# Optimization experiments

Measured on AMD Instinct MI355X. Metric: run time of the kernel, lower is better.

The kernel has to match this reference:

```python
import jax, jax.numpy as jnp
import numpy as np

B, N, H, W = 8, 16384, 64, 64
CTX, OUT, ST = 32, 2, 1
HID = [516, 256, 128, 64, 32, 16]
IN_SIZE = CTX + 2 + ST + OUT  # 37


def _bilinear_sample(img, coord):
    """torch F.grid_sample, mode=bilinear, padding=zeros, align_corners=False.
    img: [B,C,H,W]; coord: [B,N,2] (x,y in [-1,1]). Returns [B,C,N]."""
    _, _, Hh, Ww = img.shape
    gx = (coord[..., 0] + 1.0) * (Ww * 0.5) - 0.5
    gy = (coord[..., 1] + 1.0) * (Hh * 0.5) - 0.5
    x0 = jnp.floor(gx)
    y0 = jnp.floor(gy)
    wx1 = gx - x0
    wy1 = gy - y0

    def tap(xi, yi, w):
        valid = (xi >= 0) & (xi < Ww) & (yi >= 0) & (yi < Hh)
        xc = jnp.clip(xi, 0, Ww - 1).astype(jnp.int32)
        yc = jnp.clip(yi, 0, Hh - 1).astype(jnp.int32)
        vals = jax.vmap(lambda im, y, x: im[:, y, x])(img, yc, xc)  # [B,C,N]
        return vals * (w * valid)[:, None, :]

    return (tap(x0, y0, (1 - wx1) * (1 - wy1))
            + tap(x0 + 1, y0, wx1 * (1 - wy1))
            + tap(x0, y0 + 1, (1 - wx1) * wy1)
            + tap(x0 + 1, y0 + 1, wx1 * wy1))


def _layer_shapes():
    shapes = [(IN_SIZE, HID[0])]
    for i in range(len(HID) - 1):
        shapes.append((HID[i] + IN_SIZE, HID[i + 1]))
    shapes.append((HID[-1], OUT))
    return shapes


def setup_inputs():
    key = jax.random.key(0)
    ks = jax.random.split(key, 4 + 7)
    inp = {
        "lr_fields": jax.random.normal(ks[0], (B, OUT, H, W), jnp.float32),
        "context_grid": jax.random.normal(ks[1], (B, CTX, H, W), jnp.float32),
        "hr_eps": jax.random.normal(ks[2], (B, H, W), jnp.float32),
        "coord": jax.random.uniform(ks[3], (B, N, 2), jnp.float32, -1.0, 1.0),
    }
    for j, (fi, fo) in enumerate(_layer_shapes()):
        inp[f"W{j}"] = jax.random.normal(ks[4 + j], (fi, fo), jnp.float32) / np.sqrt(fi)
        inp[f"b{j}"] = jnp.zeros((fo,), jnp.float32)
    return inp


def reference(lr_fields, context_grid, hr_eps, coord,
              W0, b0, W1, b1, W2, b2, W3, b3, W4, b4, W5, b5, W6, b6):
    # original permutes (0,1,3,2) before grid_sample -> swap spatial axes
    ctx_pts = _bilinear_sample(jnp.swapaxes(context_grid, 2, 3), coord)  # [B,CTX,N]
    lr_pts = _bilinear_sample(jnp.swapaxes(lr_fields, 2, 3), coord)      # [B,OUT,N]
    eps_pts = _bilinear_sample(jnp.swapaxes(hr_eps[:, None], 2, 3), coord)  # [B,1,N]
    x_in = jnp.concatenate([
        jnp.transpose(ctx_pts, (0, 2, 1)),
        coord,
        jnp.transpose(lr_pts, (0, 2, 1)),
        jnp.transpose(eps_pts, (0, 2, 1)),
    ], axis=2)  # [B,N,37]
    x = jax.nn.relu(x_in @ W0 + b0)
    for Wl, bl in ((W1, b1), (W2, b2), (W3, b3), (W4, b4), (W5, b5)):
        x = jax.nn.relu(jnp.concatenate([x, x_in], axis=2) @ Wl + bl)
    return x @ W6 + b6  # [B,N,2]
```

## Files before the change

kernel.cpp:

```cpp
#include <hip/hip_runtime.h>


#define NTH     1024
#define NWAVES  16
#define MPTS    32
#define MTILES  (MPTS / 16)
#define SROW    872
#define XIN_OFF 0
#define HA_OFF  64
#define HB_OFF  608
#define NPOINTS (8 * 16384)
#define GRIDX   (NPOINTS / MPTS)
#define LDSBYTES (MPTS * SROW * 2)

#define SGB __builtin_amdgcn_sched_group_barrier
#define SG_MFMA   0x008
#define SG_VMREAD 0x020
#define SG_DSREAD 0x100

typedef short          short8  __attribute__((ext_vector_type(8)));
typedef short          short4v __attribute__((ext_vector_type(4)));
typedef float          f32x4   __attribute__((ext_vector_type(4)));
typedef unsigned short u16;

__device__ __forceinline__ u16 f2bf(float f) {
    unsigned int u = __builtin_bit_cast(unsigned int, f);
    u += 0x7fffu + ((u >> 16) & 1u);
    return (u16)(u >> 16);
}

__constant__ int pk_base8[8] = {0, 4224, 23680, 28800, 30336, 30848, 31040, 31104};
__constant__ int pk_ks[7]    = {2, 19, 10, 6, 4, 3, 1};
__constant__ int pk_khp[7]   = {0, 544, 256, 128, 64, 32, 32};
__constant__ int pk_kact[7]  = {0, 516, 256, 128, 64, 32, 16};
__constant__ int pk_nact[7]  = {516, 256, 128, 64, 32, 16, 2};

struct WPtrs { const float* W[7]; };

__global__ void pack_weights(WPtrs wp, u16* __restrict__ out)
{
    const int f = blockIdx.x * blockDim.x + threadIdx.x;
    if (f >= 31104) return;
    int l = 0;
    while (l < 6 && f >= pk_base8[l + 1]) ++l;
    const int r    = f - pk_base8[l];
    const int lane = r & 63;
    const int t    = r >> 6;
    const int ks   = pk_ks[l];
    const int s    = t % ks;
    const int nt   = t / ks;
    const int n    = nt * 16 + (lane & 15);
    const int k0   = s * 32 + (lane >> 4) * 8;
    const int nact = pk_nact[l];
    const int khp  = pk_khp[l];
    const int kact = pk_kact[l];
    const float* W = wp.W[l];

    union { short8 v; u16 e[8]; } frag;
#pragma unroll
    for (int j = 0; j < 8; ++j) {
        const int k = k0 + j;
        float v = 0.0f;
        if (n < nact) {
            if (k < khp) {
                if (k < kact) v = W[k * nact + n];
            } else {
                const int xr = k - khp;
                if (xr < 37) v = W[(kact + xr) * nact + n];
            }
        }
        frag.e[j] = f2bf(v);
    }
    *(short8*)(out + (size_t)f * 8) = frag.v;
}

template<int KHP, int HSEG, int OSEG, int NT, int NACT, int LBASE,
         bool XIN, bool RELU, bool GOUT>
__device__ __forceinline__ void mlayer(const u16* __restrict__ wpack,
                                       const float* __restrict__ bias,
                                       u16* __restrict__ s_act,
                                       float* __restrict__ gout, int p0,
                                       int wave, int lane)
{
    constexpr int KHS = KHP / 32;
    constexpr int KS  = KHS + (XIN ? 2 : 0);
    constexpr int MS  = MTILES;
    const int lm = lane & 15;
    const int lq = lane >> 4;
    const u16* wl = wpack + LBASE + lane * 8;

    const u16* arow[MS];
#pragma unroll
    for (int m = 0; m < MS; ++m)
        arow[m] = s_act + (m * 16 + lm) * SROW + lq * 8;

    for (int nt = wave; nt < NT; nt += NWAVES) {
        const u16* bp = wl + (size_t)nt * KS * 512;

        f32x4 acc[MS];
#pragma unroll
        for (int m = 0; m < MS; ++m)
            acc[m] = (f32x4){0.f, 0.f, 0.f, 0.f};

#pragma unroll
        for (int s = 0; s < KS; ++s) {
            const int ab = (s < KHS) ? (HSEG + s * 32)
                                     : (XIN_OFF + (s - KHS) * 32);
            short8 a[MS];
#pragma unroll
            for (int m = 0; m < MS; ++m)
                a[m] = *(const short8*)(arow[m] + ab);
            const short8 b = *(const short8*)(bp + (size_t)s * 512);
#pragma unroll
            for (int m = 0; m < MS; ++m)
                acc[m] = __builtin_amdgcn_mfma_f32_16x16x32_bf16(b, a[m], acc[m], 0, 0, 0);
        }

        SGB(SG_DSREAD, 2, 0); SGB(SG_VMREAD, 1, 0);
        if (KS > 1) { SGB(SG_DSREAD, 2, 0); SGB(SG_VMREAD, 1, 0); }
#pragma unroll
        for (int s = 0; s < KS; ++s) {
            SGB(SG_MFMA, 2, 0);
            if (s + 2 < KS) { SGB(SG_DSREAD, 2, 0); SGB(SG_VMREAD, 1, 0); }
        }

        const int bn = nt * 16 + lq * 4;
        float bv[4];
        if (bn + 4 <= NACT) {
            const f32x4 b4 = *(const f32x4*)(bias + bn);
            bv[0] = b4[0]; bv[1] = b4[1]; bv[2] = b4[2]; bv[3] = b4[3];
        } else {
#pragma unroll
            for (int r = 0; r < 4; ++r)
                bv[r] = (bn + r < NACT) ? bias[bn + r] : 0.f;
        }
        if (GOUT) {
            if (lq == 0) {
#pragma unroll
                for (int m = 0; m < MS; ++m) {
                    float2 o;
                    o.x = acc[m][0] + bv[0];
                    o.y = acc[m][1] + bv[1];
                    *(float2*)(gout + (size_t)(p0 + m * 16 + lm) * 2) = o;
                }
            }
        } else {
#pragma unroll
            for (int m = 0; m < MS; ++m) {
                short4v o;
#pragma unroll
                for (int r = 0; r < 4; ++r) {
                    float v = acc[m][r] + bv[r];
                    if (RELU) v = fmaxf(v, 0.f);
                    o[r] = (short)f2bf(v);
                }
                *(short4v*)(s_act + (size_t)(m * 16 + lm) * SROW + OSEG + bn) = o;
            }
        }
    }
}

struct MainParams {
    const float* lr;
    const float* ctx;
    const float* eps;
    const float* coord;
    const float* Bb[7];
    const u16*   wpack;
    float*       out;
};

__global__ __launch_bounds__(NTH, 8)
void cont_decoder_mfma(MainParams p)
{
    extern __shared__ u16 s_act[];
    __shared__ int   s_x0[MPTS], s_y0[MPTS];
    __shared__ float s_wx[MPTS], s_wy[MPTS];

    const int tid  = threadIdx.x;
    const int wave = tid >> 6;
    const int lane = tid & 63;
    const int p0   = blockIdx.x * MPTS;
    const int b    = p0 >> 14;

    for (int i = tid; i < MPTS * 43; i += NTH) {
        const int pt = i / 43, c = i % 43;
        const int col = (c < 27) ? (37 + c) : (592 + (c - 27));
        s_act[pt * SROW + col] = 0;
    }

    if (tid < MPTS) {
        const int pt = p0 + tid;
        const float cx = p.coord[2 * pt];
        const float cy = p.coord[2 * pt + 1];
        const float gx = (cx + 1.0f) * 32.0f - 0.5f;
        const float gy = (cy + 1.0f) * 32.0f - 0.5f;
        const float fx0 = floorf(gx), fy0 = floorf(gy);
        s_x0[tid] = (int)fx0;
        s_y0[tid] = (int)fy0;
        s_wx[tid] = gx - fx0;
        s_wy[tid] = gy - fy0;
        s_act[tid * SROW + 32] = f2bf(cx);
        s_act[tid * SROW + 33] = f2bf(cy);
    }
    __syncthreads();

    for (int idx = tid; idx < MPTS * 35; idx += NTH) {
        const int t = idx / 35;
        const int c = idx % 35;
        const float* base;
        int col;
        if (c < 32)      { base = p.ctx + (size_t)(b * 32 + c) * 4096;       col = c; }
        else if (c < 34) { base = p.lr  + (size_t)(b * 2 + (c - 32)) * 4096; col = 34 + (c - 32); }
        else             { base = p.eps + (size_t)b * 4096;                   col = 36; }

        const int   x0 = s_x0[t], y0 = s_y0[t];
        const float wx = s_wx[t], wy = s_wy[t];
        const int x1 = x0 + 1, y1 = y0 + 1;
        const bool xv0 = (x0 >= 0) & (x0 < 64);
        const bool xv1 = (x1 >= 0) & (x1 < 64);
        const bool yv0 = (y0 >= 0) & (y0 < 64);
        const bool yv1 = (y1 >= 0) & (y1 < 64);
        const int xc0 = min(max(x0, 0), 63), xc1 = min(max(x1, 0), 63);
        const int yc0 = min(max(y0, 0), 63), yc1 = min(max(y1, 0), 63);

        const float w00 = (1.0f - wx) * (1.0f - wy) * ((xv0 && yv0) ? 1.0f : 0.0f);
        const float w10 = wx * (1.0f - wy)          * ((xv1 && yv0) ? 1.0f : 0.0f);
        const float w01 = (1.0f - wx) * wy          * ((xv0 && yv1) ? 1.0f : 0.0f);
        const float w11 = wx * wy                   * ((xv1 && yv1) ? 1.0f : 0.0f);

        const float val = w00 * base[xc0 * 64 + yc0]
                        + w10 * base[xc1 * 64 + yc0]
                        + w01 * base[xc0 * 64 + yc1]
                        + w11 * base[xc1 * 64 + yc1];
        s_act[t * SROW + col] = f2bf(val);
    }
    __syncthreads();

    mlayer<  0,  HA_OFF, HA_OFF, 33, 516, 0,      true,  true,  false>(p.wpack, p.Bb[0], s_act, nullptr, p0, wave, lane);
    __syncthreads();
    mlayer<544,  HA_OFF, HB_OFF, 16, 256, 33792,  true,  true,  false>(p.wpack, p.Bb[1], s_act, nullptr, p0, wave, lane);
    __syncthreads();
    mlayer<256,  HB_OFF, HA_OFF,  8, 128, 189440, true,  true,  false>(p.wpack, p.Bb[2], s_act, nullptr, p0, wave, lane);
    __syncthreads();
    mlayer<128,  HA_OFF, HB_OFF,  4,  64, 230400, true,  true,  false>(p.wpack, p.Bb[3], s_act, nullptr, p0, wave, lane);
    __syncthreads();
    mlayer< 64,  HB_OFF, HA_OFF,  2,  32, 242688, true,  true,  false>(p.wpack, p.Bb[4], s_act, nullptr, p0, wave, lane);
    __syncthreads();
    mlayer< 32,  HA_OFF, HB_OFF,  1,  16, 246784, true,  true,  false>(p.wpack, p.Bb[5], s_act, nullptr, p0, wave, lane);
    __syncthreads();
    mlayer< 32,  HB_OFF, 0,       1,   2, 248320, false, false, true >(p.wpack, p.Bb[6], s_act, p.out,   p0, wave, lane);
}

extern "C" void kernel_launch(void* const* d_in, const int* in_sizes, int n_in,
                              void* d_out, int out_size, void* d_ws, size_t ws_size,
                              hipStream_t stream)
{
    WPtrs wp;
    for (int l = 0; l < 7; ++l) wp.W[l] = (const float*)d_in[4 + 2 * l];

    MainParams p;
    p.lr    = (const float*)d_in[0];
    p.ctx   = (const float*)d_in[1];
    p.eps   = (const float*)d_in[2];
    p.coord = (const float*)d_in[3];
    for (int l = 0; l < 7; ++l) p.Bb[l] = (const float*)d_in[5 + 2 * l];
    p.wpack = (const u16*)d_ws;
    p.out   = (float*)d_out;

    hipFuncSetAttribute((const void*)cont_decoder_mfma,
                        hipFuncAttributeMaxDynamicSharedMemorySize, LDSBYTES);

    hipLaunchKernelGGL(pack_weights, dim3(122), dim3(256), 0, stream, wp, (u16*)d_ws);
    hipLaunchKernelGGL(cont_decoder_mfma, dim3(GRIDX), dim3(NTH), LDSBYTES, stream, p);
}
```

Measured before the change: 220.8 us.

## Split K across wave halves for layers 1-2 with LDS partial-sum reduction

For the 256- and 128-wide layers, which had fewer N-tiles than waves and left half the waves idle, the K dimension is now split across two groups of eight waves. Each wave owns NT/8 column tiles, the second group writes fp32 partial sums into an unused LDS region, and the first group adds them, applies bias and ReLU, and stores bf16 activations. The manual sched_group_barrier interleaving hints are also removed. This costs extra barriers, LDS scratch traffic and more accumulator registers per wave.

```diff
diff --git a/kernel.cpp b/kernel.cpp
--- a/kernel.cpp
+++ b/kernel.cpp
@@ -6,17 +6,13 @@
 #define MPTS    32
 #define MTILES  (MPTS / 16)
 #define SROW    872
+#define SROWB   (SROW * 2)
 #define XIN_OFF 0
 #define HA_OFF  64
 #define HB_OFF  608
 #define NPOINTS (8 * 16384)
 #define GRIDX   (NPOINTS / MPTS)
 #define LDSBYTES (MPTS * SROW * 2)
-
-#define SGB __builtin_amdgcn_sched_group_barrier
-#define SG_MFMA   0x008
-#define SG_VMREAD 0x020
-#define SG_DSREAD 0x100
 
 typedef short          short8  __attribute__((ext_vector_type(8)));
 typedef short          short4v __attribute__((ext_vector_type(4)));
@@ -75,7 +71,7 @@
 }
 
 template<int KHP, int HSEG, int OSEG, int NT, int NACT, int LBASE,
-         bool XIN, bool RELU, bool GOUT>
+         int KSPLIT, int SCRB, bool BAR1, bool XIN, bool RELU, bool GOUT>
 __device__ __forceinline__ void mlayer(const u16* __restrict__ wpack,
                                        const float* __restrict__ bias,
                                        u16* __restrict__ s_act,
@@ -94,67 +90,149 @@
     for (int m = 0; m < MS; ++m)
         arow[m] = s_act + (m * 16 + lm) * SROW + lq * 8;
 
-    for (int nt = wave; nt < NT; nt += NWAVES) {
-        const u16* bp = wl + (size_t)nt * KS * 512;
-
-        f32x4 acc[MS];
-#pragma unroll
-        for (int m = 0; m < MS; ++m)
-            acc[m] = (f32x4){0.f, 0.f, 0.f, 0.f};
-
-#pragma unroll
-        for (int s = 0; s < KS; ++s) {
-            const int ab = (s < KHS) ? (HSEG + s * 32)
-                                     : (XIN_OFF + (s - KHS) * 32);
-            short8 a[MS];
+    if constexpr (KSPLIT == 1) {
+        for (int nt = wave; nt < NT; nt += NWAVES) {
+            const u16* bp = wl + (size_t)nt * KS * 512;
+
+            f32x4 acc[MS];
 #pragma unroll
             for (int m = 0; m < MS; ++m)
-                a[m] = *(const short8*)(arow[m] + ab);
-            const short8 b = *(const short8*)(bp + (size_t)s * 512);
+                acc[m] = (f32x4){0.f, 0.f, 0.f, 0.f};
+
+#pragma unroll
+            for (int s = 0; s < KS; ++s) {
+                const int ab = (s < KHS) ? (HSEG + s * 32)
+                                         : (XIN_OFF + (s - KHS) * 32);
+                short8 a[MS];
+#pragma unroll
+                for (int m = 0; m < MS; ++m)
+                    a[m] = *(const short8*)(arow[m] + ab);
+                const short8 b = *(const short8*)(bp + (size_t)s * 512);
+#pragma unroll
+                for (int m = 0; m < MS; ++m)
+                    acc[m] = __builtin_amdgcn_mfma_f32_16x16x32_bf16(b, a[m], acc[m], 0, 0, 0);
+            }
+
+            const int bn = nt * 16 + lq * 4;
+            float bv[4];
+            if (bn + 4 <= NACT) {
+                const f32x4 b4 = *(const f32x4*)(bias + bn);
+                bv[0] = b4[0]; bv[1] = b4[1]; bv[2] = b4[2]; bv[3] = b4[3];
+            } else {
+#pragma unroll
+                for (int r = 0; r < 4; ++r)
+                    bv[r] = (bn + r < NACT) ? bias[bn + r] : 0.f;
+            }
+            if (GOUT) {
+                if (lq == 0) {
+#pragma unroll
+                    for (int m = 0; m < MS; ++m) {
+                        float2 o;
+                        o.x = acc[m][0] + bv[0];
+                        o.y = acc[m][1] + bv[1];
+                        *(float2*)(gout + (size_t)(p0 + m * 16 + lm) * 2) = o;
+                    }
+                }
+            } else {
+#pragma unroll
+                for (int m = 0; m < MS; ++m) {
+                    short4v o;
+#pragma unroll
+                    for (int r = 0; r < 4; ++r) {
+                        float v = acc[m][r] + bv[r];
+                        if (RELU) v = fmaxf(v, 0.f);
+                        o[r] = (short)f2bf(v);
+                    }
+                    *(short4v*)(s_act + (size_t)(m * 16 + lm) * SROW + OSEG + bn) = o;
+                }
+            }
+        }
+    } else {
+        constexpr int NTN  = NT / 8;
+        constexpr int SMID = (KS + 1) / 2;
+        const int q  = wave & 7;
+        const int kh = wave >> 3;
+
+        const u16* bp[NTN];
+#pragma unroll
+        for (int i = 0; i < NTN; ++i)
+            bp[i] = wl + (size_t)(q + 8 * i) * KS * 512;
+
+        f32x4 acc[NTN][MS];
+#pragma unroll
+        for (int i = 0; i < NTN; ++i)
 #pragma unroll
             for (int m = 0; m < MS; ++m)
-                acc[m] = __builtin_amdgcn_mfma_f32_16x16x32_bf16(b, a[m], acc[m], 0, 0, 0);
-        }
-
-        SGB(SG_DSREAD, 2, 0); SGB(SG_VMREAD, 1, 0);
-        if (KS > 1) { SGB(SG_DSREAD, 2, 0); SGB(SG_VMREAD, 1, 0); }
-#pragma unroll
-        for (int s = 0; s < KS; ++s) {
-            SGB(SG_MFMA, 2, 0);
-            if (s + 2 < KS) { SGB(SG_DSREAD, 2, 0); SGB(SG_VMREAD, 1, 0); }
-        }
-
-        const int bn = nt * 16 + lq * 4;
-        float bv[4];
-        if (bn + 4 <= NACT) {
-            const f32x4 b4 = *(const f32x4*)(bias + bn);
-            bv[0] = b4[0]; bv[1] = b4[1]; bv[2] = b4[2]; bv[3] = b4[3];
+                acc[i][m] = (f32x4){0.f, 0.f, 0.f, 0.f};
+
+#define KSTEP(s_) { \
+            const int ab = ((s_) < KHS) ? (HSEG + (s_) * 32) \
+                                        : (XIN_OFF + ((s_) - KHS) * 32); \
+            short8 a[MS]; \
+            for (int m = 0; m < MS; ++m) \
+                a[m] = *(const short8*)(arow[m] + ab); \
+            for (int i = 0; i < NTN; ++i) { \
+                const short8 b = *(const short8*)(bp[i] + (size_t)(s_) * 512); \
+                for (int m = 0; m < MS; ++m) \
+                    acc[i][m] = __builtin_amdgcn_mfma_f32_16x16x32_bf16(b, a[m], acc[i][m], 0, 0, 0); \
+            } }
+
+        if (kh == 0) {
+#pragma unroll
+            for (int s = 0; s < SMID; ++s) KSTEP(s)
         } else {
 #pragma unroll
-            for (int r = 0; r < 4; ++r)
-                bv[r] = (bn + r < NACT) ? bias[bn + r] : 0.f;
-        }
-        if (GOUT) {
-            if (lq == 0) {
+            for (int s = SMID; s < KS; ++s) KSTEP(s)
+        }
+#undef KSTEP
+
+        if constexpr (BAR1) __syncthreads();
+        if (kh == 1) {
+#pragma unroll
+            for (int i = 0; i < NTN; ++i) {
+                const int nt = q + 8 * i;
 #pragma unroll
                 for (int m = 0; m < MS; ++m) {
-                    float2 o;
-                    o.x = acc[m][0] + bv[0];
-                    o.y = acc[m][1] + bv[1];
-                    *(float2*)(gout + (size_t)(p0 + m * 16 + lm) * 2) = o;
-                }
-            }
-        } else {
-#pragma unroll
-            for (int m = 0; m < MS; ++m) {
-                short4v o;
-#pragma unroll
-                for (int r = 0; r < 4; ++r) {
-                    float v = acc[m][r] + bv[r];
-                    if (RELU) v = fmaxf(v, 0.f);
-                    o[r] = (short)f2bf(v);
-                }
-                *(short4v*)(s_act + (size_t)(m * 16 + lm) * SROW + OSEG + bn) = o;
+                    char* sp = (char*)s_act + (size_t)(m * 16 + lm) * SROWB
+                             + SCRB + nt * 64 + lq * 16;
+                    *(f32x4*)sp = acc[i][m];
+                }
+            }
+        }
+        __syncthreads();
+        if (kh == 0) {
+#pragma unroll
+            for (int i = 0; i < NTN; ++i) {
+                const int nt = q + 8 * i;
+#pragma unroll
+                for (int m = 0; m < MS; ++m) {
+                    const char* sp = (const char*)s_act
+                                   + (size_t)(m * 16 + lm) * SROWB
+                                   + SCRB + nt * 64 + lq * 16;
+                    acc[i][m] += *(const f32x4*)sp;
+                }
+
+                const int bn = nt * 16 + lq * 4;
+                float bv[4];
+                if (bn + 4 <= NACT) {
+                    const f32x4 b4 = *(const f32x4*)(bias + bn);
+                    bv[0] = b4[0]; bv[1] = b4[1]; bv[2] = b4[2]; bv[3] = b4[3];
+                } else {
+#pragma unroll
+                    for (int r = 0; r < 4; ++r)
+                        bv[r] = (bn + r < NACT) ? bias[bn + r] : 0.f;
+                }
+#pragma unroll
+                for (int m = 0; m < MS; ++m) {
+                    short4v o;
+#pragma unroll
+                    for (int r = 0; r < 4; ++r) {
+                        float v = acc[i][m][r] + bv[r];
+                        if (RELU) v = fmaxf(v, 0.f);
+                        o[r] = (short)f2bf(v);
+                    }
+                    *(short4v*)(s_act + (size_t)(m * 16 + lm) * SROW + OSEG + bn) = o;
+                }
             }
         }
     }
@@ -237,19 +315,19 @@
     }
     __syncthreads();
 
-    mlayer<  0,  HA_OFF, HA_OFF, 33, 516, 0,      true,  true,  false>(p.wpack, p.Bb[0], s_act, nullptr, p0, wave, lane);
-    __syncthreads();
-    mlayer<544,  HA_OFF, HB_OFF, 16, 256, 33792,  true,  true,  false>(p.wpack, p.Bb[1], s_act, nullptr, p0, wave, lane);
-    __syncthreads();
-    mlayer<256,  HB_OFF, HA_OFF,  8, 128, 189440, true,  true,  false>(p.wpack, p.Bb[2], s_act, nullptr, p0, wave, lane);
-    __syncthreads();
-    mlayer<128,  HA_OFF, HB_OFF,  4,  64, 230400, true,  true,  false>(p.wpack, p.Bb[3], s_act, nullptr, p0, wave, lane);
-    __syncthreads();
-    mlayer< 64,  HB_OFF, HA_OFF,  2,  32, 242688, true,  true,  false>(p.wpack, p.Bb[4], s_act, nullptr, p0, wave, lane);
-    __syncthreads();
-    mlayer< 32,  HA_OFF, HB_OFF,  1,  16, 246784, true,  true,  false>(p.wpack, p.Bb[5], s_act, nullptr, p0, wave, lane);
-    __syncthreads();
-    mlayer< 32,  HB_OFF, 0,       1,   2, 248320, false, false, true >(p.wpack, p.Bb[6], s_act, p.out,   p0, wave, lane);
+    mlayer<  0,  HA_OFF, HA_OFF, 33, 516, 0,      1,  0,    false, true,  true,  false>(p.wpack, p.Bb[0], s_act, nullptr, p0, wave, lane);
+    __syncthreads();
+    mlayer<544,  HA_OFF, HB_OFF, 16, 256, 33792,  2,  128,  true,  true,  true,  false>(p.wpack, p.Bb[1], s_act, nullptr, p0, wave, lane);
+    __syncthreads();
+    mlayer<256,  HB_OFF, HA_OFF,  8, 128, 189440, 2,  640,  false, true,  true,  false>(p.wpack, p.Bb[2], s_act, nullptr, p0, wave, lane);
+    __syncthreads();
+    mlayer<128,  HA_OFF, HB_OFF,  4,  64, 230400, 1,  0,    false, true,  true,  false>(p.wpack, p.Bb[3], s_act, nullptr, p0, wave, lane);
+    __syncthreads();
+    mlayer< 64,  HB_OFF, HA_OFF,  2,  32, 242688, 1,  0,    false, true,  true,  false>(p.wpack, p.Bb[4], s_act, nullptr, p0, wave, lane);
+    __syncthreads();
+    mlayer< 32,  HA_OFF, HB_OFF,  1,  16, 246784, 1,  0,    false, true,  true,  false>(p.wpack, p.Bb[5], s_act, nullptr, p0, wave, lane);
+    __syncthreads();
+    mlayer< 32,  HB_OFF, 0,       1,   2, 248320, 1,  0,    false, false, false, true >(p.wpack, p.Bb[6], s_act, p.out,   p0, wave, lane);
 }
 
 extern "C" void kernel_launch(void* const* d_in, const int* in_sizes, int n_in,
```

Measured after the change: 225.4 us. 2.1% more time.

## Switch MLP layers from 16x16x32 to 32x32x16 bf16 MFMA with repacked weights

Applied to the files above, without the earlier changes.

Replaces the two 16x16x32 MFMAs per K-step (one per 16-point M tile) with a single 32x32x16 MFMA covering all 32 points and 32 output columns. The weight packing and layer offsets are redone for 32-column fragments with 16-wide K slices, and the manual sched_group_barrier hints are removed. This halves the number of N tiles per layer, which reduces redundant LDS A reads and per-tile epilogue work. The cost is more padding waste on small layers (e.g. the 16- and 2-wide outputs), fewer N tiles to spread across 16 waves, and dropping the explicit instruction interleaving.

```diff
diff --git a/kernel.cpp b/kernel.cpp
--- a/kernel.cpp
+++ b/kernel.cpp
@@ -4,7 +4,6 @@
 #define NTH     1024
 #define NWAVES  16
 #define MPTS    32
-#define MTILES  (MPTS / 16)
 #define SROW    872
 #define XIN_OFF 0
 #define HA_OFF  64
@@ -13,14 +12,10 @@
 #define GRIDX   (NPOINTS / MPTS)
 #define LDSBYTES (MPTS * SROW * 2)
 
-#define SGB __builtin_amdgcn_sched_group_barrier
-#define SG_MFMA   0x008
-#define SG_VMREAD 0x020
-#define SG_DSREAD 0x100
-
 typedef short          short8  __attribute__((ext_vector_type(8)));
 typedef short          short4v __attribute__((ext_vector_type(4)));
 typedef float          f32x4   __attribute__((ext_vector_type(4)));
+typedef float          f32x16  __attribute__((ext_vector_type(16)));
 typedef unsigned short u16;
 
 __device__ __forceinline__ u16 f2bf(float f) {
@@ -29,34 +24,34 @@
     return (u16)(u >> 16);
 }
 
-__constant__ int pk_base8[8] = {0, 4224, 23680, 28800, 30336, 30848, 31040, 31104};
-__constant__ int pk_ks[7]    = {2, 19, 10, 6, 4, 3, 1};
-__constant__ int pk_khp[7]   = {0, 544, 256, 128, 64, 32, 32};
-__constant__ int pk_kact[7]  = {0, 516, 256, 128, 64, 32, 16};
-__constant__ int pk_nact[7]  = {516, 256, 128, 64, 32, 16, 2};
+__constant__ int pk_base[8] = {0, 68, 372, 452, 476, 484, 490, 492};
+__constant__ int pk_ks[7]   = {4, 38, 20, 12, 8, 6, 2};
+__constant__ int pk_khp[7]  = {0, 544, 256, 128, 64, 32, 32};
+__constant__ int pk_kact[7] = {0, 516, 256, 128, 64, 32, 16};
+__constant__ int pk_nact[7] = {516, 256, 128, 64, 32, 16, 2};
 
 struct WPtrs { const float* W[7]; };
 
 __global__ void pack_weights(WPtrs wp, u16* __restrict__ out)
 {
-    const int f = blockIdx.x * blockDim.x + threadIdx.x;
-    if (f >= 31104) return;
+    const int t = blockIdx.x * blockDim.x + threadIdx.x;
+    if (t >= 492 * 64) return;
+    const int frag = t >> 6;
+    const int lane = t & 63;
     int l = 0;
-    while (l < 6 && f >= pk_base8[l + 1]) ++l;
-    const int r    = f - pk_base8[l];
-    const int lane = r & 63;
-    const int t    = r >> 6;
+    while (l < 6 && frag >= pk_base[l + 1]) ++l;
+    const int r    = frag - pk_base[l];
     const int ks   = pk_ks[l];
-    const int s    = t % ks;
-    const int nt   = t / ks;
-    const int n    = nt * 16 + (lane & 15);
-    const int k0   = s * 32 + (lane >> 4) * 8;
+    const int s    = r % ks;
+    const int nt   = r / ks;
+    const int n    = nt * 32 + (lane & 31);
+    const int k0   = s * 16 + (lane >> 5) * 8;
     const int nact = pk_nact[l];
     const int khp  = pk_khp[l];
     const int kact = pk_kact[l];
     const float* W = wp.W[l];
 
-    union { short8 v; u16 e[8]; } frag;
+    union { short8 v; u16 e[8]; } fr;
 #pragma unroll
     for (int j = 0; j < 8; ++j) {
         const int k = k0 + j;
@@ -69,9 +64,9 @@
                 if (xr < 37) v = W[(kact + xr) * nact + n];
             }
         }
-        frag.e[j] = f2bf(v);
-    }
-    *(short8*)(out + (size_t)f * 8) = frag.v;
+        fr.e[j] = f2bf(v);
+    }
+    *(short8*)(out + (size_t)t * 8) = fr.v;
 }
 
 template<int KHP, int HSEG, int OSEG, int NT, int NACT, int LBASE,
@@ -82,79 +77,57 @@
                                        float* __restrict__ gout, int p0,
                                        int wave, int lane)
 {
-    constexpr int KHS = KHP / 32;
-    constexpr int KS  = KHS + (XIN ? 2 : 0);
-    constexpr int MS  = MTILES;
-    const int lm = lane & 15;
-    const int lq = lane >> 4;
-    const u16* wl = wpack + LBASE + lane * 8;
-
-    const u16* arow[MS];
-#pragma unroll
-    for (int m = 0; m < MS; ++m)
-        arow[m] = s_act + (m * 16 + lm) * SROW + lq * 8;
+    constexpr int KHS = KHP / 16;
+    constexpr int KS  = KHS + (XIN ? 4 : 0);
+    const int pt = lane & 31;
+    const int hl = lane >> 5;
+    const u16* wl   = wpack + LBASE + lane * 8;
+    const u16* arow = s_act + pt * SROW + hl * 8;
 
     for (int nt = wave; nt < NT; nt += NWAVES) {
         const u16* bp = wl + (size_t)nt * KS * 512;
 
-        f32x4 acc[MS];
-#pragma unroll
-        for (int m = 0; m < MS; ++m)
-            acc[m] = (f32x4){0.f, 0.f, 0.f, 0.f};
+        f32x16 acc;
+#pragma unroll
+        for (int i = 0; i < 16; ++i) acc[i] = 0.f;
 
 #pragma unroll
         for (int s = 0; s < KS; ++s) {
-            const int ab = (s < KHS) ? (HSEG + s * 32)
-                                     : (XIN_OFF + (s - KHS) * 32);
-            short8 a[MS];
-#pragma unroll
-            for (int m = 0; m < MS; ++m)
-                a[m] = *(const short8*)(arow[m] + ab);
+            const int ab = (s < KHS) ? (HSEG + s * 16)
+                                     : (XIN_OFF + (s - KHS) * 16);
+            const short8 a = *(const short8*)(arow + ab);
             const short8 b = *(const short8*)(bp + (size_t)s * 512);
-#pragma unroll
-            for (int m = 0; m < MS; ++m)
-                acc[m] = __builtin_amdgcn_mfma_f32_16x16x32_bf16(b, a[m], acc[m], 0, 0, 0);
+            acc = __builtin_amdgcn_mfma_f32_32x32x16_bf16(b, a, acc, 0, 0, 0);
         }
 
-        SGB(SG_DSREAD, 2, 0); SGB(SG_VMREAD, 1, 0);
-        if (KS > 1) { SGB(SG_DSREAD, 2, 0); SGB(SG_VMREAD, 1, 0); }
-#pragma unroll
-        for (int s = 0; s < KS; ++s) {
-            SGB(SG_MFMA, 2, 0);
-            if (s + 2 < KS) { SGB(SG_DSREAD, 2, 0); SGB(SG_VMREAD, 1, 0); }
-        }
-
-        const int bn = nt * 16 + lq * 4;
-        float bv[4];
-        if (bn + 4 <= NACT) {
-            const f32x4 b4 = *(const f32x4*)(bias + bn);
-            bv[0] = b4[0]; bv[1] = b4[1]; bv[2] = b4[2]; bv[3] = b4[3];
-        } else {
-#pragma unroll
-            for (int r = 0; r < 4; ++r)
-                bv[r] = (bn + r < NACT) ? bias[bn + r] : 0.f;
-        }
         if (GOUT) {
-            if (lq == 0) {
-#pragma unroll
-                for (int m = 0; m < MS; ++m) {
-                    float2 o;
-                    o.x = acc[m][0] + bv[0];
-                    o.y = acc[m][1] + bv[1];
-                    *(float2*)(gout + (size_t)(p0 + m * 16 + lm) * 2) = o;
-                }
+            if (hl == 0) {
+                float2 o;
+                o.x = acc[0] + bias[0];
+                o.y = acc[1] + bias[1];
+                *(float2*)(gout + (size_t)(p0 + pt) * 2) = o;
             }
         } else {
 #pragma unroll
-            for (int m = 0; m < MS; ++m) {
+            for (int rq = 0; rq < 4; ++rq) {
+                const int bn = nt * 32 + rq * 8 + hl * 4;
+                float bv[4];
+                if (bn + 4 <= NACT) {
+                    const f32x4 b4 = *(const f32x4*)(bias + bn);
+                    bv[0] = b4[0]; bv[1] = b4[1]; bv[2] = b4[2]; bv[3] = b4[3];
+                } else {
+#pragma unroll
+                    for (int e = 0; e < 4; ++e)
+                        bv[e] = (bn + e < NACT) ? bias[bn + e] : 0.f;
+                }
                 short4v o;
 #pragma unroll
-                for (int r = 0; r < 4; ++r) {
-                    float v = acc[m][r] + bv[r];
+                for (int e = 0; e < 4; ++e) {
+                    float v = acc[rq * 4 + e] + bv[e];
                     if (RELU) v = fmaxf(v, 0.f);
-                    o[r] = (short)f2bf(v);
+                    o[e] = (short)f2bf(v);
                 }
-                *(short4v*)(s_act + (size_t)(m * 16 + lm) * SROW + OSEG + bn) = o;
+                *(short4v*)(s_act + (size_t)pt * SROW + OSEG + bn) = o;
             }
         }
     }
@@ -237,19 +210,19 @@
     }
     __syncthreads();
 
-    mlayer<  0,  HA_OFF, HA_OFF, 33, 516, 0,      true,  true,  false>(p.wpack, p.Bb[0], s_act, nullptr, p0, wave, lane);
-    __syncthreads();
-    mlayer<544,  HA_OFF, HB_OFF, 16, 256, 33792,  true,  true,  false>(p.wpack, p.Bb[1], s_act, nullptr, p0, wave, lane);
-    __syncthreads();
-    mlayer<256,  HB_OFF, HA_OFF,  8, 128, 189440, true,  true,  false>(p.wpack, p.Bb[2], s_act, nullptr, p0, wave, lane);
-    __syncthreads();
-    mlayer<128,  HA_OFF, HB_OFF,  4,  64, 230400, true,  true,  false>(p.wpack, p.Bb[3], s_act, nullptr, p0, wave, lane);
-    __syncthreads();
-    mlayer< 64,  HB_OFF, HA_OFF,  2,  32, 242688, true,  true,  false>(p.wpack, p.Bb[4], s_act, nullptr, p0, wave, lane);
-    __syncthreads();
-    mlayer< 32,  HA_OFF, HB_OFF,  1,  16, 246784, true,  true,  false>(p.wpack, p.Bb[5], s_act, nullptr, p0, wave, lane);
-    __syncthreads();
-    mlayer< 32,  HB_OFF, 0,       1,   2, 248320, false, false, true >(p.wpack, p.Bb[6], s_act, p.out,   p0, wave, lane);
+    mlayer<  0,  HA_OFF, HA_OFF, 17, 516, 0,       true,  true,  false>(p.wpack, p.Bb[0], s_act, nullptr, p0, wave, lane);
+    __syncthreads();
+    mlayer<544,  HA_OFF, HB_OFF,  8, 256, 34816,   true,  true,  false>(p.wpack, p.Bb[1], s_act, nullptr, p0, wave, lane);
+    __syncthreads();
+    mlayer<256,  HB_OFF, HA_OFF,  4, 128, 190464,  true,  true,  false>(p.wpack, p.Bb[2], s_act, nullptr, p0, wave, lane);
+    __syncthreads();
+    mlayer<128,  HA_OFF, HB_OFF,  2,  64, 231424,  true,  true,  false>(p.wpack, p.Bb[3], s_act, nullptr, p0, wave, lane);
+    __syncthreads();
+    mlayer< 64,  HB_OFF, HA_OFF,  1,  32, 243712,  true,  true,  false>(p.wpack, p.Bb[4], s_act, nullptr, p0, wave, lane);
+    __syncthreads();
+    mlayer< 32,  HA_OFF, HB_OFF,  1,  16, 247808,  true,  true,  false>(p.wpack, p.Bb[5], s_act, nullptr, p0, wave, lane);
+    __syncthreads();
+    mlayer< 32,  HB_OFF, 0,       1,   2, 250880,  false, false, true >(p.wpack, p.Bb[6], s_act, p.out,   p0, wave, lane);
 }
 
 extern "C" void kernel_launch(void* const* d_in, const int* in_sizes, int n_in,
@@ -271,6 +244,6 @@
     hipFuncSetAttribute((const void*)cont_decoder_mfma,
                         hipFuncAttributeMaxDynamicSharedMemorySize, LDSBYTES);
 
-    hipLaunchKernelGGL(pack_weights, dim3(122), dim3(256), 0, stream, wp, (u16*)d_ws);
+    hipLaunchKernelGGL(pack_weights, dim3(123), dim3(256), 0, stream, wp, (u16*)d_ws);
     hipLaunchKernelGGL(cont_decoder_mfma, dim3(GRIDX), dim3(NTH), LDSBYTES, stream, p);
 }
```

Result: slower. 227.4 us (+3.0%).

## Prefetch next layer's first weight fragments across barriers, merge sampling setup

Applied to the files above, without the earlier changes.

Before each inter-layer barrier, every wave issues global loads for the first two weight fragments of its first tile in the next layer. The first tile then uses these registers, so weight-fetch latency overlaps the barrier wait. The separate coordinate-setup pass and its barrier are removed: each sampling thread recomputes the bilinear indices from coord itself. The explicit sched_group_barrier interleaving hints are also dropped, which hands instruction scheduling back to the compiler and may change how MFMA and memory reads overlap.

```diff
diff --git a/kernel.cpp b/kernel.cpp
--- a/kernel.cpp
+++ b/kernel.cpp
@@ -13,15 +13,13 @@
 #define GRIDX   (NPOINTS / MPTS)
 #define LDSBYTES (MPTS * SROW * 2)
 
-#define SGB __builtin_amdgcn_sched_group_barrier
-#define SG_MFMA   0x008
-#define SG_VMREAD 0x020
-#define SG_DSREAD 0x100
-
 typedef short          short8  __attribute__((ext_vector_type(8)));
 typedef short          short4v __attribute__((ext_vector_type(4)));
 typedef float          f32x4   __attribute__((ext_vector_type(4)));
 typedef unsigned short u16;
+
+struct TrueT  { static constexpr bool value = true;  };
+struct FalseT { static constexpr bool value = false; };
 
 __device__ __forceinline__ u16 f2bf(float f) {
     unsigned int u = __builtin_bit_cast(unsigned int, f);
@@ -74,13 +72,28 @@
     *(short8*)(out + (size_t)f * 8) = frag.v;
 }
 
+struct PF2 { short8 b0, b1; };
+
+template<int KS, int LBASE, int NT>
+__device__ __forceinline__ PF2 prefetch(const u16* __restrict__ wpack,
+                                        int wave, int lane)
+{
+    PF2 pf;
+    if (wave < NT) {
+        const u16* bp = wpack + LBASE + lane * 8 + (size_t)wave * KS * 512;
+        pf.b0 = *(const short8*)(bp);
+        if constexpr (KS > 1) pf.b1 = *(const short8*)(bp + 512);
+    }
+    return pf;
+}
+
 template<int KHP, int HSEG, int OSEG, int NT, int NACT, int LBASE,
          bool XIN, bool RELU, bool GOUT>
 __device__ __forceinline__ void mlayer(const u16* __restrict__ wpack,
                                        const float* __restrict__ bias,
                                        u16* __restrict__ s_act,
                                        float* __restrict__ gout, int p0,
-                                       int wave, int lane)
+                                       int wave, int lane, const PF2 pf)
 {
     constexpr int KHS = KHP / 32;
     constexpr int KS  = KHS + (XIN ? 2 : 0);
@@ -94,7 +107,8 @@
     for (int m = 0; m < MS; ++m)
         arow[m] = s_act + (m * 16 + lm) * SROW + lq * 8;
 
-    for (int nt = wave; nt < NT; nt += NWAVES) {
+    auto unit = [&](int nt, auto usepf) {
+        constexpr bool USEPF = decltype(usepf)::value;
         const u16* bp = wl + (size_t)nt * KS * 512;
 
         f32x4 acc[MS];
@@ -110,18 +124,16 @@
 #pragma unroll
             for (int m = 0; m < MS; ++m)
                 a[m] = *(const short8*)(arow[m] + ab);
-            const short8 b = *(const short8*)(bp + (size_t)s * 512);
+            short8 b;
+            bool got = false;
+            if constexpr (USEPF) {
+                if (s == 0) { b = pf.b0; got = true; }
+                if constexpr (KS > 1) { if (s == 1) { b = pf.b1; got = true; } }
+            }
+            if (!got) b = *(const short8*)(bp + (size_t)s * 512);
 #pragma unroll
             for (int m = 0; m < MS; ++m)
                 acc[m] = __builtin_amdgcn_mfma_f32_16x16x32_bf16(b, a[m], acc[m], 0, 0, 0);
-        }
-
-        SGB(SG_DSREAD, 2, 0); SGB(SG_VMREAD, 1, 0);
-        if (KS > 1) { SGB(SG_DSREAD, 2, 0); SGB(SG_VMREAD, 1, 0); }
-#pragma unroll
-        for (int s = 0; s < KS; ++s) {
-            SGB(SG_MFMA, 2, 0);
-            if (s + 2 < KS) { SGB(SG_DSREAD, 2, 0); SGB(SG_VMREAD, 1, 0); }
         }
 
         const int bn = nt * 16 + lq * 4;
@@ -157,6 +169,12 @@
                 *(short4v*)(s_act + (size_t)(m * 16 + lm) * SROW + OSEG + bn) = o;
             }
         }
+    };
+
+    if (wave < NT) {
+        unit(wave, TrueT{});
+        for (int nt = wave + NWAVES; nt < NT; nt += NWAVES)
+            unit(nt, FalseT{});
     }
 }
 
@@ -174,8 +192,6 @@
 void cont_decoder_mfma(MainParams p)
 {
     extern __shared__ u16 s_act[];
-    __shared__ int   s_x0[MPTS], s_y0[MPTS];
-    __shared__ float s_wx[MPTS], s_wy[MPTS];
 
     const int tid  = threadIdx.x;
     const int wave = tid >> 6;
@@ -189,33 +205,31 @@
         s_act[pt * SROW + col] = 0;
     }
 
-    if (tid < MPTS) {
-        const int pt = p0 + tid;
+    for (int idx = tid; idx < MPTS * 36; idx += NTH) {
+        const int t = idx / 36;
+        const int c = idx % 36;
+        const int pt = p0 + t;
         const float cx = p.coord[2 * pt];
         const float cy = p.coord[2 * pt + 1];
+
+        if (c == 35) {
+            s_act[t * SROW + 32] = f2bf(cx);
+            s_act[t * SROW + 33] = f2bf(cy);
+            continue;
+        }
+
         const float gx = (cx + 1.0f) * 32.0f - 0.5f;
         const float gy = (cy + 1.0f) * 32.0f - 0.5f;
         const float fx0 = floorf(gx), fy0 = floorf(gy);
-        s_x0[tid] = (int)fx0;
-        s_y0[tid] = (int)fy0;
-        s_wx[tid] = gx - fx0;
-        s_wy[tid] = gy - fy0;
-        s_act[tid * SROW + 32] = f2bf(cx);
-        s_act[tid * SROW + 33] = f2bf(cy);
-    }
-    __syncthreads();
-
-    for (int idx = tid; idx < MPTS * 35; idx += NTH) {
-        const int t = idx / 35;
-        const int c = idx % 35;
+        const int   x0 = (int)fx0,  y0 = (int)fy0;
+        const float wx = gx - fx0,  wy = gy - fy0;
+
         const float* base;
         int col;
         if (c < 32)      { base = p.ctx + (size_t)(b * 32 + c) * 4096;       col = c; }
         else if (c < 34) { base = p.lr  + (size_t)(b * 2 + (c - 32)) * 4096; col = 34 + (c - 32); }
         else             { base = p.eps + (size_t)b * 4096;                   col = 36; }
 
-        const int   x0 = s_x0[t], y0 = s_y0[t];
-        const float wx = s_wx[t], wy = s_wy[t];
         const int x1 = x0 + 1, y1 = y0 + 1;
         const bool xv0 = (x0 >= 0) & (x0 < 64);
         const bool xv1 = (x1 >= 0) & (x1 < 64);
@@ -235,21 +249,28 @@
                         + w11 * base[xc1 * 64 + yc1];
         s_act[t * SROW + col] = f2bf(val);
     }
-    __syncthreads();
-
-    mlayer<  0,  HA_OFF, HA_OFF, 33, 516, 0,      true,  true,  false>(p.wpack, p.Bb[0], s_act, nullptr, p0, wave, lane);
-    __syncthreads();
-    mlayer<544,  HA_OFF, HB_OFF, 16, 256, 33792,  true,  true,  false>(p.wpack, p.Bb[1], s_act, nullptr, p0, wave, lane);
-    __syncthreads();
-    mlayer<256,  HB_OFF, HA_OFF,  8, 128, 189440, true,  true,  false>(p.wpack, p.Bb[2], s_act, nullptr, p0, wave, lane);
-    __syncthreads();
-    mlayer<128,  HA_OFF, HB_OFF,  4,  64, 230400, true,  true,  false>(p.wpack, p.Bb[3], s_act, nullptr, p0, wave, lane);
-    __syncthreads();
-    mlayer< 64,  HB_OFF, HA_OFF,  2,  32, 242688, true,  true,  false>(p.wpack, p.Bb[4], s_act, nullptr, p0, wave, lane);
-    __syncthreads();
-    mlayer< 32,  HA_OFF, HB_OFF,  1,  16, 246784, true,  true,  false>(p.wpack, p.Bb[5], s_act, nullptr, p0, wave, lane);
-    __syncthreads();
-    mlayer< 32,  HB_OFF, 0,       1,   2, 248320, false, false, true >(p.wpack, p.Bb[6], s_act, p.out,   p0, wave, lane);
+
+    PF2 pf = prefetch< 2, 0,      33>(p.wpack, wave, lane);
+    __syncthreads();
+    mlayer<  0,  HA_OFF, HA_OFF, 33, 516, 0,      true,  true,  false>(p.wpack, p.Bb[0], s_act, nullptr, p0, wave, lane, pf);
+    pf = prefetch<19, 33792, 16>(p.wpack, wave, lane);
+    __syncthreads();
+    mlayer<544,  HA_OFF, HB_OFF, 16, 256, 33792,  true,  true,  false>(p.wpack, p.Bb[1], s_act, nullptr, p0, wave, lane, pf);
+    pf = prefetch<10, 189440, 8>(p.wpack, wave, lane);
+    __syncthreads();
+    mlayer<256,  HB_OFF, HA_OFF,  8, 128, 189440, true,  true,  false>(p.wpack, p.Bb[2], s_act, nullptr, p0, wave, lane, pf);
+    pf = prefetch< 6, 230400, 4>(p.wpack, wave, lane);
+    __syncthreads();
+    mlayer<128,  HA_OFF, HB_OFF,  4,  64, 230400, true,  true,  false>(p.wpack, p.Bb[3], s_act, nullptr, p0, wave, lane, pf);
+    pf = prefetch< 4, 242688, 2>(p.wpack, wave, lane);
+    __syncthreads();
+    mlayer< 64,  HB_OFF, HA_OFF,  2,  32, 242688, true,  true,  false>(p.wpack, p.Bb[4], s_act, nullptr, p0, wave, lane, pf);
+    pf = prefetch< 3, 246784, 1>(p.wpack, wave, lane);
+    __syncthreads();
+    mlayer< 32,  HA_OFF, HB_OFF,  1,  16, 246784, true,  true,  false>(p.wpack, p.Bb[5], s_act, nullptr, p0, wave, lane, pf);
+    pf = prefetch< 1, 248320, 1>(p.wpack, wave, lane);
+    __syncthreads();
+    mlayer< 32,  HB_OFF, 0,       1,   2, 248320, false, false, true >(p.wpack, p.Bb[6], s_act, p.out,   p0, wave, lane, pf);
 }
 
 extern "C" void kernel_launch(void* const* d_in, const int* in_sizes, int n_in,
```

New measurement: 227.5 us. +3.0%, slower.
